# Kernel tuning notes

Hardware: AMD Instinct MI355X
Metric: run time of the kernel (lower is better)

Reference implementation:

```python
import jax, jax.numpy as jnp
import numpy as np

NUM_HEADS = 16
EPS = 1e-6
CHUNK = 128  # chunk length for exact chunked-recurrent causal linear attention


def setup_inputs() -> dict:
    key = jax.random.key(0)
    ks = jax.random.split(key, 6)
    B, T, E = 4, 2048, 1024
    s = 0.02
    x = jax.random.normal(ks[0], (B, T, E), jnp.float32)
    Wq = jax.random.normal(ks[1], (E, E), jnp.float32) * s
    Wk = jax.random.normal(ks[2], (E, E), jnp.float32) * s
    Wv = jax.random.normal(ks[3], (E, E), jnp.float32) * s
    Wp = jax.random.normal(ks[4], (E, E), jnp.float32) * s
    bp = jnp.zeros((E,), jnp.float32)
    return {"x": x, "Wq": Wq, "Wk": Wk, "Wv": Wv, "Wp": Wp, "bp": bp}


def reference(x, Wq, Wk, Wv, Wp, bp):
    B, T, E = x.shape
    H = NUM_HEADS
    D = E // H
    N = T // CHUNK

    q = x @ Wq.T
    k = x @ Wk.T
    v = x @ Wv.T

    def split_heads(t):  # [B,T,E] -> [B,H,N,C,D]
        return t.reshape(B, T, H, D).transpose(0, 2, 1, 3).reshape(B, H, N, CHUNK, D)

    phi_q = jax.nn.elu(split_heads(q)) + 1.0
    phi_k = jax.nn.elu(split_heads(k)) + 1.0
    vh = split_heads(v)

    # per-chunk KV state and key-sum, then exclusive prefix over chunks
    kv = jnp.einsum('bhncd,bhnce->bhnde', phi_k, vh)        # [B,H,N,D,D]
    zk = phi_k.sum(axis=3)                                   # [B,H,N,D]
    S_prev = jnp.concatenate(
        [jnp.zeros_like(kv[:, :, :1]), jnp.cumsum(kv, axis=2)[:, :, :-1]], axis=2)
    Z_prev = jnp.concatenate(
        [jnp.zeros_like(zk[:, :, :1]), jnp.cumsum(zk, axis=2)[:, :, :-1]], axis=2)

    # intra-chunk causal part
    A = jnp.einsum('bhncd,bhnsd->bhncs', phi_q, phi_k)       # [B,H,N,C,C]
    mask = jnp.tril(jnp.ones((CHUNK, CHUNK), bool))
    A = jnp.where(mask, A, 0.0)

    num = (jnp.einsum('bhncs,bhnse->bhnce', A, vh)
           + jnp.einsum('bhncd,bhnde->bhnce', phi_q, S_prev))
    den = A.sum(-1) + jnp.einsum('bhncd,bhnd->bhnc', phi_q, Z_prev) + EPS
    y = num / den[..., None]                                  # [B,H,N,C,D]

    y = y.reshape(B, H, T, D).transpose(0, 2, 1, 3).reshape(B, T, E)
    return y @ Wp.T + bp
```

## Files before the change

### kernel.cpp

```cpp
#include <hip/hip_runtime.h>
#include <hip/hip_bf16.h>
#include <stdint.h>

#define T_LEN  2048
#define E_DIM  1024
#define BATCH  4
#define HEADS  16
#define HDIM   64
#define CHUNK_ 128
#define NCHUNK 16
#define EPS_   1e-6f

typedef __attribute__((ext_vector_type(8))) short bf16x8;
typedef __attribute__((ext_vector_type(4))) float f32x4;

__device__ __forceinline__ float b2f(__hip_bfloat16 h) { return __bfloat162float(h); }
__device__ __forceinline__ unsigned short f2bu(float f) {
  __hip_bfloat16 h = __float2bfloat16(f);
  return *(unsigned short*)&h;
}
__device__ __forceinline__ void gld_lds16(const void* g, void* l) {
  __builtin_amdgcn_global_load_lds((const __attribute__((address_space(1))) void*)g,
                                   (__attribute__((address_space(3))) void*)l,
                                   16, 0, 0);
}

#define MFMA16(a, b, c) __builtin_amdgcn_mfma_f32_16x16x32_bf16((a), (b), (c), 0, 0, 0)

__global__ __launch_bounds__(256)
void cast5(const float* __restrict__ x,  const float* __restrict__ w0,
           const float* __restrict__ w1, const float* __restrict__ w2,
           const float* __restrict__ w3,
           __hip_bfloat16* __restrict__ xb,  __hip_bfloat16* __restrict__ w0b,
           __hip_bfloat16* __restrict__ w1b, __hip_bfloat16* __restrict__ w2b,
           __hip_bfloat16* __restrict__ w3b)
{
  const int b = blockIdx.x;
  const float* s;
  __hip_bfloat16* d;
  size_t off;
  if (b < 8192) { s = x; d = xb; off = (size_t)b * 1024; }
  else {
    const int i = (b - 8192) >> 10;
    const int r = (b - 8192) & 1023;
    s = (i == 0) ? w0 : (i == 1) ? w1 : (i == 2) ? w2 : w3;
    d = (i == 0) ? w0b : (i == 1) ? w1b : (i == 2) ? w2b : w3b;
    off = (size_t)r * 1024;
  }
  const int t = threadIdx.x;
  float4 v = *(const float4*)(s + off + (size_t)t * 4);
  ushort4 o;
  o.x = f2bu(v.x); o.y = f2bu(v.y); o.z = f2bu(v.z); o.w = f2bu(v.w);
  *(ushort4*)((unsigned short*)d + off + (size_t)t * 4) = o;
}

__device__ __forceinline__ void gemm128_core(
    const __hip_bfloat16* __restrict__ X,
    const __hip_bfloat16* __restrict__ W,
    int bm, int bn, f32x4 acc[4][4],
    __hip_bfloat16* Xs, __hip_bfloat16* Ws)
{
  const int t = threadIdx.x, lane = t & 63, wave = t >> 6;
  const int wm = (wave >> 1) * 64, wn = (wave & 1) * 64;
  for (int k0 = 0; k0 < 1024; k0 += 32) {
    if (k0) __syncthreads();
#pragma unroll
    for (int i = 0; i < 2; ++i) {
      const int j = wave * 2 + i;
      const int m = j * 16 + (lane >> 2);
      const int kg = lane & 3;
      gld_lds16(X + (size_t)(bm * 128 + m) * 1024 + k0 + kg * 8, (char*)Xs + j * 1024);
      gld_lds16(W + (size_t)(bn * 128 + m) * 1024 + k0 + kg * 8, (char*)Ws + j * 1024);
    }
    __syncthreads();
    bf16x8 a[4], b[4];
#pragma unroll
    for (int i = 0; i < 4; ++i) {
      a[i] = *(const bf16x8*)&Xs[((wm + i * 16 + (lane & 15)) * 4 + (lane >> 4)) * 8];
      b[i] = *(const bf16x8*)&Ws[((wn + i * 16 + (lane & 15)) * 4 + (lane >> 4)) * 8];
    }
#pragma unroll
    for (int i = 0; i < 4; ++i)
#pragma unroll
      for (int jn = 0; jn < 4; ++jn)
        acc[i][jn] = MFMA16(a[i], b[jn], acc[i][jn]);
  }
}

__global__ __launch_bounds__(512, 1)
void gemm_qkv_v2(const __hip_bfloat16* __restrict__ X,
                 const __hip_bfloat16* __restrict__ Wq,
                 const __hip_bfloat16* __restrict__ Wk,
                 const __hip_bfloat16* __restrict__ Wv,
                 __hip_bfloat16* __restrict__ qo,
                 __hip_bfloat16* __restrict__ ko,
                 __hip_bfloat16* __restrict__ vo)
{
  __shared__ __align__(16) unsigned short As[3][8192];
  __shared__ __align__(16) unsigned short Bs[3][16384];

  const int bm = blockIdx.x;
  const int byy = blockIdx.y;
  const int which = byy >> 2, bn = byy & 3;
  const __hip_bfloat16* Wsel = (which == 0) ? Wq : (which == 1) ? Wk : Wv;
  __hip_bfloat16* Cc = (which == 0) ? qo : (which == 1) ? ko : vo;
  const bool elu = (which < 2);

  const int t = threadIdx.x, lane = t & 63, wv = t >> 6;
  const int wm = (wv >> 2) * 64;
  const int wn = (wv & 3) * 64;

  const __hip_bfloat16* Xp = X + (size_t)(bm * 128) * 1024;
  const __hip_bfloat16* Wp = Wsel + (size_t)(bn * 256) * 1024;

  const int lo    = (lane & 15) * 128;
  const int lohi0 = lo + (((lane >> 4)    ) ^ (lane & 7)) * 16;
  const int lohi1 = lo + (((lane >> 4) | 4) ^ (lane & 7)) * 16;
  const int srow = lane >> 3;
  const int scg  = (lane & 7) ^ (lane >> 3);

  auto stA = [&](int buf, int k0) {
#pragma unroll
    for (int ci = 0; ci < 2; ++ci) {
      const int row0 = (wv * 2 + ci) * 8;
      gld_lds16(Xp + (size_t)(row0 + srow) * 1024 + k0 + scg * 8,
                (char*)&As[buf][0] + row0 * 128);
    }
  };
  auto stB0 = [&](int buf, int k0) {
#pragma unroll
    for (int ci = 0; ci < 2; ++ci) {
      const int row0 = (wv * 2 + ci) * 8;
      gld_lds16(Wp + (size_t)(row0 + srow) * 1024 + k0 + scg * 8,
                (char*)&Bs[buf][0] + row0 * 128);
    }
  };
  auto stB1 = [&](int buf, int k0) {
#pragma unroll
    for (int ci = 0; ci < 2; ++ci) {
      const int row0 = 128 + (wv * 2 + ci) * 8;
      gld_lds16(Wp + (size_t)(row0 + srow) * 1024 + k0 + scg * 8,
                (char*)&Bs[buf][0] + row0 * 128);
    }
  };
  auto rdA = [&](int buf, int half, bf16x8 (&d)[2][2]) {
#pragma unroll
    for (int m = 0; m < 2; ++m) {
      const int rb = wm + half * 32 + m * 16;
      d[m][0] = *(const bf16x8*)((const char*)&As[buf][0] + rb * 128 + lohi0);
      d[m][1] = *(const bf16x8*)((const char*)&As[buf][0] + rb * 128 + lohi1);
    }
  };
  auto rdB = [&](int buf, int half, bf16x8 (&d)[2][2]) {
#pragma unroll
    for (int n = 0; n < 2; ++n) {
      const int rb = wn + half * 32 + n * 16;
      d[n][0] = *(const bf16x8*)((const char*)&Bs[buf][0] + rb * 128 + lohi0);
      d[n][1] = *(const bf16x8*)((const char*)&Bs[buf][0] + rb * 128 + lohi1);
    }
  };

  f32x4 acc[4][4];
#pragma unroll
  for (int m = 0; m < 4; ++m)
#pragma unroll
    for (int n = 0; n < 4; ++n) acc[m][n] = (f32x4){0.f, 0.f, 0.f, 0.f};

  bf16x8 Aa01[2][2], Ab01[2][2], Aa23[2][2], Ab23[2][2];
  bf16x8 Ba01[2][2], Bb01[2][2], Ba23[2][2], Bb23[2][2];

  stA(0, 0);  stB0(0, 0);  stB1(0, 0);
  stA(1, 64); stB0(1, 64); stB1(1, 64);
  asm volatile("s_waitcnt vmcnt(6)" ::: "memory");
  __builtin_amdgcn_s_barrier();
  __builtin_amdgcn_sched_barrier(0);
  rdA(0, 0, Aa01); rdB(0, 0, Ab01); rdA(0, 1, Aa23); rdB(0, 1, Ab23);

  auto qstep = [&](int j, int c,
                   bf16x8 (&ca01)[2][2], bf16x8 (&cb01)[2][2],
                   bf16x8 (&ca23)[2][2], bf16x8 (&cb23)[2][2],
                   bf16x8 (&na01)[2][2], bf16x8 (&nb01)[2][2],
                   bf16x8 (&na23)[2][2], bf16x8 (&nb23)[2][2]) {
    const int stg  = (c + 2 >= 3) ? c - 1 : c + 2;
    const int nbuf = (c + 1 >= 3) ? 0 : c + 1;
    const int k0n  = (j + 2) * 64;
    const bool dost = (j < 14);

    __builtin_amdgcn_s_setprio(1);
#pragma unroll
    for (int m = 0; m < 2; ++m)
#pragma unroll
      for (int n = 0; n < 2; ++n) {
        acc[m][n] = MFMA16(ca01[m][0], cb01[n][0], acc[m][n]);
        acc[m][n] = MFMA16(ca01[m][1], cb01[n][1], acc[m][n]);
      }
    __builtin_amdgcn_s_setprio(0);
    if (dost) stA(stg, k0n);

    __builtin_amdgcn_s_setprio(1);
#pragma unroll
    for (int m = 0; m < 2; ++m)
#pragma unroll
      for (int n = 0; n < 2; ++n) {
        acc[m][2 + n] = MFMA16(ca01[m][0], cb23[n][0], acc[m][2 + n]);
        acc[m][2 + n] = MFMA16(ca01[m][1], cb23[n][1], acc[m][2 + n]);
      }
    __builtin_amdgcn_s_setprio(0);
    if (dost) stB0(stg, k0n);

    __builtin_amdgcn_s_setprio(1);
#pragma unroll
    for (int m = 0; m < 2; ++m)
#pragma unroll
      for (int n = 0; n < 2; ++n) {
        acc[2 + m][n] = MFMA16(ca23[m][0], cb01[n][0], acc[2 + m][n]);
        acc[2 + m][n] = MFMA16(ca23[m][1], cb01[n][1], acc[2 + m][n]);
      }
    __builtin_amdgcn_s_setprio(0);
    if (dost) stB1(stg, k0n);

    if (j == 14) asm volatile("s_waitcnt vmcnt(0)" ::: "memory");
    else         asm volatile("s_waitcnt vmcnt(6)" ::: "memory");
    __builtin_amdgcn_s_barrier();
    __builtin_amdgcn_sched_barrier(0);

    rdA(nbuf, 0, na01); rdB(nbuf, 0, nb01);

    __builtin_amdgcn_s_setprio(1);
#pragma unroll
    for (int m = 0; m < 2; ++m)
#pragma unroll
      for (int n = 0; n < 2; ++n) {
        acc[2 + m][2 + n] = MFMA16(ca23[m][0], cb23[n][0], acc[2 + m][2 + n]);
        acc[2 + m][2 + n] = MFMA16(ca23[m][1], cb23[n][1], acc[2 + m][2 + n]);
      }
    __builtin_amdgcn_s_setprio(0);

    rdA(nbuf, 1, na23); rdB(nbuf, 1, nb23);
  };

  int c = 0;
#pragma unroll 1
  for (int jj = 0; jj < 8; ++jj) {
    qstep(2 * jj, c, Aa01, Ab01, Aa23, Ab23, Ba01, Bb01, Ba23, Bb23);
    c = (c == 2) ? 0 : c + 1;
    qstep(2 * jj + 1, c, Ba01, Bb01, Ba23, Bb23, Aa01, Ab01, Aa23, Ab23);
    c = (c == 2) ? 0 : c + 1;
  }

  const int lm = lane & 15;
  const int r0 = (lane >> 4) * 4;
#pragma unroll
  for (int m = 0; m < 4; ++m) {
    const int row = bm * 128 + wm + m * 16 + r0;
#pragma unroll
    for (int n = 0; n < 4; ++n) {
      const int col = bn * 256 + wn + n * 16 + lm;
#pragma unroll
      for (int r = 0; r < 4; ++r) {
        float vv = acc[m][n][r];
        if (elu) vv = (vv > 0.f) ? (vv + 1.f) : __expf(vv);
        Cc[(size_t)(row + r) * 1024 + col] = __float2bfloat16(vv);
      }
    }
  }
}

__global__ __launch_bounds__(256, 2)
void gemm_out(const __hip_bfloat16* __restrict__ X,
              const __hip_bfloat16* __restrict__ W,
              const float* __restrict__ bias,
              float* __restrict__ C)
{
  __shared__ __align__(16) __hip_bfloat16 Xs[128 * 32];
  __shared__ __align__(16) __hip_bfloat16 Ws[128 * 32];
  const int bm = blockIdx.x, bn = blockIdx.y;
  f32x4 acc[4][4];
#pragma unroll
  for (int i = 0; i < 4; ++i)
#pragma unroll
    for (int j = 0; j < 4; ++j) acc[i][j] = (f32x4){0.f, 0.f, 0.f, 0.f};
  gemm128_core(X, W, bm, bn, acc, Xs, Ws);
  const int lane = threadIdx.x & 63, wave = threadIdx.x >> 6;
  const int wm = (wave >> 1) * 64, wn = (wave & 1) * 64;
  const int r0 = (lane >> 4) * 4;
#pragma unroll
  for (int mi = 0; mi < 4; ++mi)
#pragma unroll
    for (int ni = 0; ni < 4; ++ni) {
      const int row = bm * 128 + wm + mi * 16 + r0;
      const int col = bn * 128 + wn + ni * 16 + (lane & 15);
      const float bv = bias[col];
#pragma unroll
      for (int r = 0; r < 4; ++r)
        C[(size_t)(row + r) * 1024 + col] = acc[mi][ni][r] + bv;
    }
}

__global__ __launch_bounds__(256)
void chunk_kv(const __hip_bfloat16* __restrict__ Kp,
              const __hip_bfloat16* __restrict__ Vp,
              float* __restrict__ kvout, float* __restrict__ zkout,
              unsigned short* __restrict__ vimg)
{
  const int bid = blockIdx.x;
  const int n = bid & 15, h = (bid >> 4) & 15, b = bid >> 8;
  __shared__ __align__(16) __hip_bfloat16 ks[CHUNK_ * HDIM];
  __shared__ __align__(16) __hip_bfloat16 vs[CHUNK_ * HDIM];
  const size_t base = ((size_t)(b * T_LEN + n * CHUNK_)) * E_DIM + h * HDIM;
  const int t = threadIdx.x;
  for (int i = t; i < CHUNK_ * 8; i += 256) {
    int r = i >> 3, c = (i & 7) << 3;
    *(uint4*)&ks[r * HDIM + c] = *(const uint4*)(Kp + base + (size_t)r * E_DIM + c);
    *(uint4*)&vs[r * HDIM + c] = *(const uint4*)(Vp + base + (size_t)r * E_DIM + c);
  }
  __syncthreads();
  const int d0 = (t >> 4) << 2, e0 = (t & 15) << 2;
  float acc[4][4] = {{0.f}};
  float z[4] = {0.f, 0.f, 0.f, 0.f};
  for (int c = 0; c < CHUNK_; ++c) {
    float kv4[4], vv4[4];
#pragma unroll
    for (int i = 0; i < 4; ++i) kv4[i] = b2f(ks[c * HDIM + d0 + i]);
#pragma unroll
    for (int j = 0; j < 4; ++j) vv4[j] = b2f(vs[c * HDIM + e0 + j]);
#pragma unroll
    for (int i = 0; i < 4; ++i) {
      z[i] += kv4[i];
#pragma unroll
      for (int j = 0; j < 4; ++j) acc[i][j] += kv4[i] * vv4[j];
    }
  }
  float* o = kvout + (size_t)bid * (HDIM * HDIM);
  const int dg = d0 >> 3, doff = d0 & 7;
#pragma unroll
  for (int i = 0; i < 4; ++i)
#pragma unroll
    for (int j = 0; j < 4; ++j)
      o[dg * 512 + (e0 + j) * 8 + doff + i] = acc[i][j];
  if (e0 == 0) {
#pragma unroll
    for (int i = 0; i < 4; ++i) zkout[(size_t)bid * HDIM + d0 + i] = z[i];
  }
  const unsigned short* vsu = (const unsigned short*)vs;
  unsigned short* vo = vimg + (size_t)bid * 8192;
  for (int slot = t; slot < 1024; slot += 256) {
    const int sg = slot >> 6, e = slot & 63;
    ushort4 lo, hi;
    lo.x = vsu[(sg * 8 + 0) * 64 + e]; lo.y = vsu[(sg * 8 + 1) * 64 + e];
    lo.z = vsu[(sg * 8 + 2) * 64 + e]; lo.w = vsu[(sg * 8 + 3) * 64 + e];
    hi.x = vsu[(sg * 8 + 4) * 64 + e]; hi.y = vsu[(sg * 8 + 5) * 64 + e];
    hi.z = vsu[(sg * 8 + 6) * 64 + e]; hi.w = vsu[(sg * 8 + 7) * 64 + e];
    *(ushort4*)&vo[slot * 8] = lo;
    *(ushort4*)&vo[slot * 8 + 4] = hi;
  }
}

__global__ __launch_bounds__(256)
void prefix_chunks(float* __restrict__ S, float* __restrict__ Z)
{
  const int bh = blockIdx.x;
  const int t = threadIdx.x;
  float run[16];
#pragma unroll
  for (int j = 0; j < 16; ++j) run[j] = 0.f;
  for (int n = 0; n < NCHUNK; ++n) {
    float* p = S + ((size_t)bh * NCHUNK + n) * (HDIM * HDIM);
#pragma unroll
    for (int j = 0; j < 16; ++j) {
      int idx = t + j * 256;
      float cur = p[idx];
      p[idx] = run[j];
      run[j] += cur;
    }
  }
  if (t < HDIM) {
    float rz = 0.f;
    for (int n = 0; n < NCHUNK; ++n) {
      float* p = Z + ((size_t)bh * NCHUNK + n) * HDIM + t;
      float cur = *p;
      *p = rz;
      rz += cur;
    }
  }
}

#define PW_STRIDE 136

__global__ __launch_bounds__(256, 3)
void chunk_attn(const __hip_bfloat16* __restrict__ Qp,
                const __hip_bfloat16* __restrict__ Kp,
                const unsigned short* __restrict__ vimg,
                const float* __restrict__ Simg,
                const float* __restrict__ Zp,
                __hip_bfloat16* __restrict__ Yp)
{
  __shared__ __align__(16) unsigned short VL[8192];
  __shared__ __align__(16) unsigned short SL[4096];
  __shared__ __align__(16) unsigned short PL[4 * 16 * PW_STRIDE];

  const int bid = blockIdx.x;
  const int n = bid & 15, h = (bid >> 4) & 15, b = bid >> 8;
  const int tokbase = b * T_LEN + n * CHUNK_;
  const size_t gbase = (size_t)tokbase * E_DIM + h * HDIM;
  const int t = threadIdx.x, lane = t & 63, wv = t >> 6;
  const int lm = lane & 15, kg = lane >> 4;

#pragma unroll
  for (int i = 0; i < 4; ++i) {
    const int j = wv * 4 + i;
    gld_lds16(vimg + (size_t)bid * 8192 + (size_t)(j * 64 + lane) * 8,
              (char*)VL + j * 1024);
  }
#pragma unroll
  for (int i = 0; i < 4; ++i) {
    const int idx = i * 1024 + t * 4;
    float4 s4 = *(const float4*)(Simg + (size_t)bid * 4096 + idx);
    ushort4 o;
    o.x = f2bu(s4.x); o.y = f2bu(s4.y); o.z = f2bu(s4.z); o.w = f2bu(s4.w);
    *(ushort4*)&SL[idx] = o;
  }

  const int mts[2] = { wv, 7 - wv };
  bf16x8 aq[2][2];
#pragma unroll
  for (int mi = 0; mi < 2; ++mi)
#pragma unroll
    for (int kh = 0; kh < 2; ++kh)
      aq[mi][kh] = *(const bf16x8*)(Qp + gbase +
                    (size_t)(mts[mi] * 16 + lm) * E_DIM + kh * 32 + kg * 8);
  bf16x8 zb[2];
#pragma unroll
  for (int kh = 0; kh < 2; ++kh) {
    float4 z0 = *(const float4*)(Zp + (size_t)bid * 64 + kh * 32 + kg * 8);
    float4 z1 = *(const float4*)(Zp + (size_t)bid * 64 + kh * 32 + kg * 8 + 4);
    zb[kh][0] = (short)f2bu(z0.x); zb[kh][1] = (short)f2bu(z0.y);
    zb[kh][2] = (short)f2bu(z0.z); zb[kh][3] = (short)f2bu(z0.w);
    zb[kh][4] = (short)f2bu(z1.x); zb[kh][5] = (short)f2bu(z1.y);
    zb[kh][6] = (short)f2bu(z1.z); zb[kh][7] = (short)f2bu(z1.w);
  }

  __syncthreads();

  f32x4 accn[2][4];
  f32x4 accden[2];
#pragma unroll
  for (int mi = 0; mi < 2; ++mi) {
    accden[mi] = (f32x4){EPS_, EPS_, EPS_, EPS_};
#pragma unroll
    for (int ne = 0; ne < 4; ++ne) accn[mi][ne] = (f32x4){0.f, 0.f, 0.f, 0.f};
  }

#pragma unroll
  for (int mi = 0; mi < 2; ++mi)
#pragma unroll
    for (int kh = 0; kh < 2; ++kh) {
      const bf16x8 a = aq[mi][kh];
      accden[mi] = MFMA16(a, zb[kh], accden[mi]);
#pragma unroll
      for (int ne = 0; ne < 4; ++ne) {
        bf16x8 bs = *(const bf16x8*)&SL[((kh * 4 + kg) * 64 + ne * 16 + lm) * 8];
        accn[mi][ne] = MFMA16(a, bs, accn[mi][ne]);
      }
    }

  unsigned short* Pw = PL + wv * 16 * PW_STRIDE;
  bf16x8 ones;
#pragma unroll
  for (int j = 0; j < 8; ++j) ones[j] = (short)0x3F80;

#pragma unroll
  for (int mi = 0; mi < 2; ++mi) {
    const int mt = mts[mi], m0 = mt * 16;
    for (int nt = 0; nt <= mt; ++nt) {
      f32x4 pt = (f32x4){0.f, 0.f, 0.f, 0.f};
#pragma unroll
      for (int kh = 0; kh < 2; ++kh) {
        bf16x8 ak = *(const bf16x8*)(Kp + gbase +
                     (size_t)(nt * 16 + lm) * E_DIM + kh * 32 + kg * 8);
        pt = MFMA16(ak, aq[mi][kh], pt);
      }
      unsigned short u[4];
#pragma unroll
      for (int r = 0; r < 4; ++r) {
        float v = pt[r];
        if (nt == mt) {
          v = ((kg * 4 + r) <= lm) ? v : 0.f;
        }
        u[r] = f2bu(v);
      }
      const int sidx = lm * PW_STRIDE + nt * 16 + kg * 4;
      *(unsigned*)&Pw[sidx]     = (unsigned)u[0] | ((unsigned)u[1] << 16);
      *(unsigned*)&Pw[sidx + 2] = (unsigned)u[2] | ((unsigned)u[3] << 16);
    }
    if ((mt & 1) == 0 && lane < 32) {
      const int m = lane >> 1, half = lane & 1;
      *(uint4*)&Pw[m * PW_STRIDE + (mt + 1) * 16 + half * 8] = (uint4){0u, 0u, 0u, 0u};
    }
    const int ktc = (mt + 2) >> 1;
    for (int kt = 0; kt < ktc; ++kt) {
      bf16x8 ap = *(const bf16x8*)&Pw[lm * PW_STRIDE + kt * 32 + kg * 8];
      accden[mi] = MFMA16(ap, ones, accden[mi]);
#pragma unroll
      for (int ne = 0; ne < 4; ++ne) {
        bf16x8 bv = *(const bf16x8*)&VL[((kt * 4 + kg) * 64 + ne * 16 + lm) * 8];
        accn[mi][ne] = MFMA16(ap, bv, accn[mi][ne]);
      }
    }
  }

#pragma unroll
  for (int mi = 0; mi < 2; ++mi) {
    const int m0 = mts[mi] * 16;
    float inv[4];
#pragma unroll
    for (int r = 0; r < 4; ++r) inv[r] = 1.f / accden[mi][r];
#pragma unroll
    for (int ne = 0; ne < 4; ++ne) {
      const int col = h * HDIM + ne * 16 + lm;
#pragma unroll
      for (int r = 0; r < 4; ++r) {
        const int row = tokbase + m0 + kg * 4 + r;
        Yp[(size_t)row * E_DIM + col] = __float2bfloat16(accn[mi][ne][r] * inv[r]);
      }
    }
  }
}

extern "C" void kernel_launch(void* const* d_in, const int* in_sizes, int n_in,
                              void* d_out, int out_size, void* d_ws, size_t ws_size,
                              hipStream_t stream)
{
  const float* x  = (const float*)d_in[0];
  const float* Wq = (const float*)d_in[1];
  const float* Wk = (const float*)d_in[2];
  const float* Wv = (const float*)d_in[3];
  const float* Wp = (const float*)d_in[4];
  const float* bp = (const float*)d_in[5];
  float* out = (float*)d_out;

  const size_t MT = (size_t)BATCH * T_LEN;
  char* w = (char*)d_ws;
  __hip_bfloat16* xb  = (__hip_bfloat16*)w; w += MT * E_DIM * sizeof(__hip_bfloat16);
  __hip_bfloat16* Wqb = (__hip_bfloat16*)w; w += (size_t)E_DIM * E_DIM * sizeof(__hip_bfloat16);
  __hip_bfloat16* Wkb = (__hip_bfloat16*)w; w += (size_t)E_DIM * E_DIM * sizeof(__hip_bfloat16);
  __hip_bfloat16* Wvb = (__hip_bfloat16*)w; w += (size_t)E_DIM * E_DIM * sizeof(__hip_bfloat16);
  __hip_bfloat16* Wpb = (__hip_bfloat16*)w; w += (size_t)E_DIM * E_DIM * sizeof(__hip_bfloat16);
  __hip_bfloat16* q = (__hip_bfloat16*)w; w += MT * E_DIM * sizeof(__hip_bfloat16);
  __hip_bfloat16* k = (__hip_bfloat16*)w; w += MT * E_DIM * sizeof(__hip_bfloat16);
  __hip_bfloat16* v = (__hip_bfloat16*)w; w += MT * E_DIM * sizeof(__hip_bfloat16);
  __hip_bfloat16* y = (__hip_bfloat16*)w; w += MT * E_DIM * sizeof(__hip_bfloat16);
  float* S = (float*)w; w += (size_t)BATCH * HEADS * NCHUNK * HDIM * HDIM * sizeof(float);
  float* Z = (float*)w; w += (size_t)BATCH * HEADS * NCHUNK * HDIM * sizeof(float);
  unsigned short* vimg = (unsigned short*)xb;

  cast5<<<8192 + 4096, 256, 0, stream>>>(x, Wq, Wk, Wv, Wp, xb, Wqb, Wkb, Wvb, Wpb);
  gemm_qkv_v2<<<dim3(64, 12), 512, 0, stream>>>(xb, Wqb, Wkb, Wvb, q, k, v);
  chunk_kv<<<BATCH * HEADS * NCHUNK, 256, 0, stream>>>(k, v, S, Z, vimg);
  prefix_chunks<<<BATCH * HEADS, 256, 0, stream>>>(S, Z);
  chunk_attn<<<BATCH * HEADS * NCHUNK, 256, 0, stream>>>(q, k, vimg, S, Z, y);
  gemm_out<<<dim3(MT / 128, 8), 256, 0, stream>>>(y, Wpb, bp, out);
}
```

Before: 245.6 us.

## Enlarge QKV GEMM tile to 256x256 with double-buffered LDS pipeline

The QKV projection GEMM moves from 128x256 tiles with a triple-buffered, register-prefetched pipeline to 256x256 tiles with double-buffered LDS. Each wave now computes a 128x64 sub-tile. Global loads for the next k-step are interleaved between MFMA groups, and a full wait plus barrier closes each step. The larger tile raises arithmetic intensity and halves the grid to 384 blocks, but it doubles the accumulator registers, keeps a 2-block occupancy hint that may not fit, and loses the cross-step register prefetch.

```diff
diff --git a/kernel.cpp b/kernel.cpp
--- a/kernel.cpp
+++ b/kernel.cpp
@@ -87,8 +87,8 @@
   }
 }
 
-__global__ __launch_bounds__(512, 1)
-void gemm_qkv_v2(const __hip_bfloat16* __restrict__ X,
+__global__ __launch_bounds__(512, 2)
+void gemm_qkv_v3(const __hip_bfloat16* __restrict__ X,
                  const __hip_bfloat16* __restrict__ Wq,
                  const __hip_bfloat16* __restrict__ Wk,
                  const __hip_bfloat16* __restrict__ Wv,
@@ -96,8 +96,8 @@
                  __hip_bfloat16* __restrict__ ko,
                  __hip_bfloat16* __restrict__ vo)
 {
-  __shared__ __align__(16) unsigned short As[3][8192];
-  __shared__ __align__(16) unsigned short Bs[3][16384];
+  __shared__ __align__(16) unsigned short As[2][16384];
+  __shared__ __align__(16) unsigned short Bs[2][16384];
 
   const int bm = blockIdx.x;
   const int byy = blockIdx.y;
@@ -107,10 +107,10 @@
   const bool elu = (which < 2);
 
   const int t = threadIdx.x, lane = t & 63, wv = t >> 6;
-  const int wm = (wv >> 2) * 64;
+  const int wm = (wv >> 2) * 128;
   const int wn = (wv & 3) * 64;
 
-  const __hip_bfloat16* Xp = X + (size_t)(bm * 128) * 1024;
+  const __hip_bfloat16* Xp = X + (size_t)(bm * 256) * 1024;
   const __hip_bfloat16* Wp = Wsel + (size_t)(bn * 256) * 1024;
 
   const int lo    = (lane & 15) * 128;
@@ -119,34 +119,20 @@
   const int srow = lane >> 3;
   const int scg  = (lane & 7) ^ (lane >> 3);
 
-  auto stA = [&](int buf, int k0) {
-#pragma unroll
-    for (int ci = 0; ci < 2; ++ci) {
-      const int row0 = (wv * 2 + ci) * 8;
-      gld_lds16(Xp + (size_t)(row0 + srow) * 1024 + k0 + scg * 8,
-                (char*)&As[buf][0] + row0 * 128);
-    }
+  auto stageA = [&](int buf, int k0, int u) {
+    const int row0 = u * 64 + wv * 8;
+    gld_lds16(Xp + (size_t)(row0 + srow) * 1024 + k0 + scg * 8,
+              (char*)&As[buf][0] + row0 * 128);
   };
-  auto stB0 = [&](int buf, int k0) {
-#pragma unroll
-    for (int ci = 0; ci < 2; ++ci) {
-      const int row0 = (wv * 2 + ci) * 8;
-      gld_lds16(Wp + (size_t)(row0 + srow) * 1024 + k0 + scg * 8,
-                (char*)&Bs[buf][0] + row0 * 128);
-    }
+  auto stageB = [&](int buf, int k0, int u) {
+    const int row0 = u * 64 + wv * 8;
+    gld_lds16(Wp + (size_t)(row0 + srow) * 1024 + k0 + scg * 8,
+              (char*)&Bs[buf][0] + row0 * 128);
   };
-  auto stB1 = [&](int buf, int k0) {
-#pragma unroll
-    for (int ci = 0; ci < 2; ++ci) {
-      const int row0 = 128 + (wv * 2 + ci) * 8;
-      gld_lds16(Wp + (size_t)(row0 + srow) * 1024 + k0 + scg * 8,
-                (char*)&Bs[buf][0] + row0 * 128);
-    }
-  };
-  auto rdA = [&](int buf, int half, bf16x8 (&d)[2][2]) {
-#pragma unroll
-    for (int m = 0; m < 2; ++m) {
-      const int rb = wm + half * 32 + m * 16;
+  auto rdA = [&](int buf, int half, bf16x8 (&d)[4][2]) {
+#pragma unroll
+    for (int m = 0; m < 4; ++m) {
+      const int rb = wm + half * 64 + m * 16;
       d[m][0] = *(const bf16x8*)((const char*)&As[buf][0] + rb * 128 + lohi0);
       d[m][1] = *(const bf16x8*)((const char*)&As[buf][0] + rb * 128 + lohi1);
     }
@@ -160,99 +146,91 @@
     }
   };
 
-  f32x4 acc[4][4];
-#pragma unroll
-  for (int m = 0; m < 4; ++m)
+  f32x4 acc[8][4];
+#pragma unroll
+  for (int m = 0; m < 8; ++m)
 #pragma unroll
     for (int n = 0; n < 4; ++n) acc[m][n] = (f32x4){0.f, 0.f, 0.f, 0.f};
 
-  bf16x8 Aa01[2][2], Ab01[2][2], Aa23[2][2], Ab23[2][2];
-  bf16x8 Ba01[2][2], Bb01[2][2], Ba23[2][2], Bb23[2][2];
-
-  stA(0, 0);  stB0(0, 0);  stB1(0, 0);
-  stA(1, 64); stB0(1, 64); stB1(1, 64);
-  asm volatile("s_waitcnt vmcnt(6)" ::: "memory");
+#pragma unroll
+  for (int u = 0; u < 4; ++u) stageA(0, 0, u);
+#pragma unroll
+  for (int u = 0; u < 4; ++u) stageB(0, 0, u);
+  asm volatile("s_waitcnt vmcnt(0)" ::: "memory");
   __builtin_amdgcn_s_barrier();
   __builtin_amdgcn_sched_barrier(0);
-  rdA(0, 0, Aa01); rdB(0, 0, Ab01); rdA(0, 1, Aa23); rdB(0, 1, Ab23);
-
-  auto qstep = [&](int j, int c,
-                   bf16x8 (&ca01)[2][2], bf16x8 (&cb01)[2][2],
-                   bf16x8 (&ca23)[2][2], bf16x8 (&cb23)[2][2],
-                   bf16x8 (&na01)[2][2], bf16x8 (&nb01)[2][2],
-                   bf16x8 (&na23)[2][2], bf16x8 (&nb23)[2][2]) {
-    const int stg  = (c + 2 >= 3) ? c - 1 : c + 2;
-    const int nbuf = (c + 1 >= 3) ? 0 : c + 1;
-    const int k0n  = (j + 2) * 64;
-    const bool dost = (j < 14);
-
+
+  auto kstep = [&](int j, int buf, bool dost) {
+    const int nbuf = buf ^ 1;
+    const int k0n  = (j + 1) * 64;
+    bf16x8 a[4][2], b0[2][2], b1[2][2];
+
+    rdA(buf, 0, a); rdB(buf, 0, b0);
+    if (dost) { stageA(nbuf, k0n, 0); stageA(nbuf, k0n, 1); stageB(nbuf, k0n, 0); }
     __builtin_amdgcn_s_setprio(1);
 #pragma unroll
-    for (int m = 0; m < 2; ++m)
+    for (int m = 0; m < 4; ++m)
 #pragma unroll
       for (int n = 0; n < 2; ++n) {
-        acc[m][n] = MFMA16(ca01[m][0], cb01[n][0], acc[m][n]);
-        acc[m][n] = MFMA16(ca01[m][1], cb01[n][1], acc[m][n]);
+        acc[m][n] = MFMA16(a[m][0], b0[n][0], acc[m][n]);
+        acc[m][n] = MFMA16(a[m][1], b0[n][1], acc[m][n]);
       }
     __builtin_amdgcn_s_setprio(0);
-    if (dost) stA(stg, k0n);
-
+
+    rdB(buf, 1, b1);
+    if (dost) { stageA(nbuf, k0n, 2); stageA(nbuf, k0n, 3); stageB(nbuf, k0n, 1); }
     __builtin_amdgcn_s_setprio(1);
 #pragma unroll
-    for (int m = 0; m < 2; ++m)
+    for (int m = 0; m < 4; ++m)
 #pragma unroll
       for (int n = 0; n < 2; ++n) {
-        acc[m][2 + n] = MFMA16(ca01[m][0], cb23[n][0], acc[m][2 + n]);
-        acc[m][2 + n] = MFMA16(ca01[m][1], cb23[n][1], acc[m][2 + n]);
+        acc[m][2 + n] = MFMA16(a[m][0], b1[n][0], acc[m][2 + n]);
+        acc[m][2 + n] = MFMA16(a[m][1], b1[n][1], acc[m][2 + n]);
       }
     __builtin_amdgcn_s_setprio(0);
-    if (dost) stB0(stg, k0n);
-
+
+    rdA(buf, 1, a);
+    if (dost) { stageB(nbuf, k0n, 2); stageB(nbuf, k0n, 3); }
     __builtin_amdgcn_s_setprio(1);
 #pragma unroll
-    for (int m = 0; m < 2; ++m)
+    for (int m = 0; m < 4; ++m)
 #pragma unroll
       for (int n = 0; n < 2; ++n) {
-        acc[2 + m][n] = MFMA16(ca23[m][0], cb01[n][0], acc[2 + m][n]);
-        acc[2 + m][n] = MFMA16(ca23[m][1], cb01[n][1], acc[2 + m][n]);
+        acc[4 + m][n] = MFMA16(a[m][0], b0[n][0], acc[4 + m][n]);
+        acc[4 + m][n] = MFMA16(a[m][1], b0[n][1], acc[4 + m][n]);
       }
     __builtin_amdgcn_s_setprio(0);
-    if (dost) stB1(stg, k0n);
-
-    if (j == 14) asm volatile("s_waitcnt vmcnt(0)" ::: "memory");
-    else         asm volatile("s_waitcnt vmcnt(6)" ::: "memory");
-    __builtin_amdgcn_s_barrier();
-    __builtin_amdgcn_sched_barrier(0);
-
-    rdA(nbuf, 0, na01); rdB(nbuf, 0, nb01);
 
     __builtin_amdgcn_s_setprio(1);
 #pragma unroll
-    for (int m = 0; m < 2; ++m)
+    for (int m = 0; m < 4; ++m)
 #pragma unroll
       for (int n = 0; n < 2; ++n) {
-        acc[2 + m][2 + n] = MFMA16(ca23[m][0], cb23[n][0], acc[2 + m][2 + n]);
-        acc[2 + m][2 + n] = MFMA16(ca23[m][1], cb23[n][1], acc[2 + m][2 + n]);
+        acc[4 + m][2 + n] = MFMA16(a[m][0], b1[n][0], acc[4 + m][2 + n]);
+        acc[4 + m][2 + n] = MFMA16(a[m][1], b1[n][1], acc[4 + m][2 + n]);
       }
     __builtin_amdgcn_s_setprio(0);
 
-    rdA(nbuf, 1, na23); rdB(nbuf, 1, nb23);
+    if (dost) {
+      asm volatile("s_waitcnt vmcnt(0)" ::: "memory");
+      __builtin_amdgcn_s_barrier();
+      __builtin_amdgcn_sched_barrier(0);
+    }
   };
 
-  int c = 0;
 #pragma unroll 1
-  for (int jj = 0; jj < 8; ++jj) {
-    qstep(2 * jj, c, Aa01, Ab01, Aa23, Ab23, Ba01, Bb01, Ba23, Bb23);
-    c = (c == 2) ? 0 : c + 1;
-    qstep(2 * jj + 1, c, Ba01, Bb01, Ba23, Bb23, Aa01, Ab01, Aa23, Ab23);
-    c = (c == 2) ? 0 : c + 1;
-  }
+  for (int jj = 0; jj < 7; ++jj) {
+    kstep(2 * jj,     0, true);
+    kstep(2 * jj + 1, 1, true);
+  }
+  kstep(14, 0, true);
+  kstep(15, 1, false);
 
   const int lm = lane & 15;
   const int r0 = (lane >> 4) * 4;
 #pragma unroll
-  for (int m = 0; m < 4; ++m) {
-    const int row = bm * 128 + wm + m * 16 + r0;
+  for (int m = 0; m < 8; ++m) {
+    const int row = bm * 256 + wm + m * 16 + r0;
 #pragma unroll
     for (int n = 0; n < 4; ++n) {
       const int col = bn * 256 + wn + n * 16 + lm;
@@ -555,7 +533,7 @@
   unsigned short* vimg = (unsigned short*)xb;
 
   cast5<<<8192 + 4096, 256, 0, stream>>>(x, Wq, Wk, Wv, Wp, xb, Wqb, Wkb, Wvb, Wpb);
-  gemm_qkv_v2<<<dim3(64, 12), 512, 0, stream>>>(xb, Wqb, Wkb, Wvb, q, k, v);
+  gemm_qkv_v3<<<dim3(32, 12), 512, 0, stream>>>(xb, Wqb, Wkb, Wvb, q, k, v);
   chunk_kv<<<BATCH * HEADS * NCHUNK, 256, 0, stream>>>(k, v, S, Z, vimg);
   prefix_chunks<<<BATCH * HEADS, 256, 0, stream>>>(S, Z);
   chunk_attn<<<BATCH * HEADS * NCHUNK, 256, 0, stream>>>(q, k, vimg, S, Z, y);
```

Result: slower. 251.2 us (+2.3%).
